# Optimization experiments

Hardware: AMD Instinct MI355X
Metric: run time of the kernel (lower is better)

The kernel has to match this reference:

```python
import jax, jax.numpy as jnp
import numpy as np

D = 256      # channels / model dim
HEADS = 8
DK = 32
DV = 32
B, H, W = 8, 32, 32
EPS = 1e-5


def setup_inputs() -> dict:
    key = jax.random.key(0)
    ks = jax.random.split(key, 9)
    s = 0.02
    return {
        "x":  jax.random.normal(ks[0], (B, D, H, W), dtype=jnp.float32),
        "Wq": jax.random.normal(ks[1], (HEADS * DK, D), dtype=jnp.float32) * s,
        "bq": jnp.zeros((HEADS * DK,), dtype=jnp.float32),
        "Wk": jax.random.normal(ks[2], (HEADS * DK, D), dtype=jnp.float32) * s,
        "bk": jnp.zeros((HEADS * DK,), dtype=jnp.float32),
        "Wv": jax.random.normal(ks[3], (HEADS * DV, D), dtype=jnp.float32) * s,
        "bv": jnp.zeros((HEADS * DV,), dtype=jnp.float32),
        "Wo": jax.random.normal(ks[4], (D, HEADS * DK), dtype=jnp.float32) * s,
        "bo": jnp.zeros((D,), dtype=jnp.float32),
    }


def reference(x, Wq, bq, Wk, bk, Wv, bv, Wo, bo):
    b, c, h, w = x.shape
    n = h * w
    # LayerNorm over [c, h, w] per sample, no affine (functional.layer_norm default)
    mu = jnp.mean(x, axis=(1, 2, 3), keepdims=True)
    var = jnp.var(x, axis=(1, 2, 3), keepdims=True)
    xn = (x - mu) * jax.lax.rsqrt(var + EPS)
    xr = xn.reshape(b, c, n).transpose(0, 2, 1)  # [b, n, c]

    def proj(Wt, bt, dh):
        y = xr @ Wt.T + bt                        # [b, n, heads*dh]
        return y.reshape(b, n, HEADS, dh).transpose(0, 2, 1, 3)  # [b, heads, n, dh]

    q = proj(Wq, bq, DK)
    k = proj(Wk, bk, DK)
    v = proj(Wv, bv, DV)

    scores = jnp.einsum('bhid,bhjd->bhij', q, k) * (DK ** -0.5)  # [b, heads, n, n]
    att = jax.nn.softmax(scores, axis=-1)
    tmp = jnp.einsum('bhij,bhjd->bhid', att, v)                  # [b, heads, n, dv]
    tmp = tmp.transpose(0, 2, 1, 3).reshape(b, n, HEADS * DV)    # [b, n, heads*dv]
    out = tmp @ Wo.T + bo                                        # [b, n, d]
    # NOTE: original does a raw .view(b, d, h, w) WITHOUT permuting — faithful reshape
    out = out.reshape(b, c, h, w)
    return out + x
```

## Files before the change

kernel.cpp:

```cpp
#include <hip/hip_runtime.h>
#include <stdint.h>

typedef unsigned short u16;
typedef unsigned int u32;
typedef __attribute__((ext_vector_type(8))) short bf16x8;
typedef __attribute__((ext_vector_type(4))) float f32x4;
typedef __attribute__((ext_vector_type(16))) float f32x16;

#define NTOK 1024
#define DMODEL 256
#define NHEAD 8
#define DK 32
#define NBATCH 8
#define PER_B (DMODEL * NTOK)

__device__ __forceinline__ float b2f(u16 h) {
    union { unsigned u; float f; } c; c.u = ((unsigned)h) << 16; return c.f;
}
__device__ __forceinline__ u16 f2b(float f) {
    unsigned u = __float_as_uint(f);
    unsigned r = u + 0x7fffu + ((u >> 16) & 1u);
    return (u16)(r >> 16);
}

__global__ void prep(const float* __restrict__ Wq, const float* __restrict__ Wk,
                     const float* __restrict__ Wv, const float* __restrict__ Wo,
                     u16* __restrict__ wb,
                     const float* __restrict__ x, float* __restrict__ part) {
    int bx = blockIdx.x;
    int t = threadIdx.x;
    if (bx < 256) {
        int m = bx >> 6;
        const float* W = (m == 0) ? Wq : (m == 1) ? Wk : (m == 2) ? Wv : Wo;
        int i = ((bx & 63) * 256 + t) * 4;
        float4 v = *(const float4*)&W[i];
        ushort4 o;
        o.x = f2b(v.x); o.y = f2b(v.y); o.z = f2b(v.z); o.w = f2b(v.w);
        *(ushort4*)&wb[m * 65536 + i] = o;
        return;
    }
    int blk = bx - 256;
    int b = blk >> 3, sl = blk & 7;
    int w = t >> 6, l = t & 63;
    const float* xb = x + (size_t)b * PER_B + sl * (PER_B / 8);
    float s = 0.f, ss = 0.f;
    for (int base = 0; base < PER_B / 8; base += 1024) {
        float4 v = *(const float4*)&xb[base + t * 4];
        s += v.x + v.y + v.z + v.w;
        ss += v.x * v.x + v.y * v.y + v.z * v.z + v.w * v.w;
    }
    for (int d = 1; d < 64; d <<= 1) {
        s += __shfl_xor(s, d, 64);
        ss += __shfl_xor(ss, d, 64);
    }
    __shared__ float red[2][4];
    if (l == 0) { red[0][w] = s; red[1][w] = ss; }
    __syncthreads();
    if (t == 0) {
        float S = red[0][0] + red[0][1] + red[0][2] + red[0][3];
        float SS = red[1][0] + red[1][1] + red[1][2] + red[1][3];
        part[(b * 8 + sl) * 2] = S;
        part[(b * 8 + sl) * 2 + 1] = SS;
    }
}

__global__ void normT(const float* __restrict__ x, const float* __restrict__ part,
                      u16* __restrict__ xn) {
    int b = blockIdx.z;
    int n0 = blockIdx.x * 32;
    int c0 = blockIdx.y * 32;
    int tx = threadIdx.x, ty = threadIdx.y;
    __shared__ float s_mu, s_rs;
    __shared__ float tile[32][33];
    if (tx == 0 && ty == 0) {
        float S = 0.f, SS = 0.f;
        for (int i = 0; i < 8; ++i) { S += part[(b * 8 + i) * 2]; SS += part[(b * 8 + i) * 2 + 1]; }
        float mu = S / (float)PER_B;
        float var = SS / (float)PER_B - mu * mu;
        s_mu = mu;
        s_rs = rsqrtf(var + 1e-5f);
    }
    __syncthreads();
    float mu = s_mu, rs = s_rs;
    const float* xb = x + (size_t)b * PER_B;
#pragma unroll
    for (int i = 0; i < 4; ++i) {
        int c = c0 + ty + i * 8;
        tile[ty + i * 8][tx] = (xb[c * NTOK + n0 + tx] - mu) * rs;
    }
    __syncthreads();
    u16* xnb = xn + (size_t)b * PER_B;
#pragma unroll
    for (int i = 0; i < 4; ++i) {
        int n = n0 + ty + i * 8;
        xnb[n * DMODEL + c0 + tx] = f2b(tile[tx][ty + i * 8]);
    }
}

__global__ __launch_bounds__(256, 4) void qkv_gemm(
    const u16* __restrict__ xn, const u16* __restrict__ wb,
    const float* __restrict__ bq, const float* __restrict__ bk,
    const float* __restrict__ bv,
    u16* __restrict__ qo, u16* __restrict__ ko, u16* __restrict__ vo) {
    int mt = blockIdx.x;
    int ot = blockIdx.y;
    int b = blockIdx.z;
    int sel = ot >> 2;
    int o0 = (ot & 3) * 64;
    const u16* W = wb + sel * 65536;
    const float* bias = (sel == 0) ? bq : (sel == 1) ? bk : bv;

    __shared__ u16 As[2][64][40];
    __shared__ u16 Bs[2][64][40];
    int t = threadIdx.x;
    int w = t >> 6, l = t & 63;
    int lr = t >> 2;
    int lc = (t & 3) * 8;
    int qd = l >> 4, ln = l & 15;

    const u16* xb = xn + ((size_t)b * NTOK + mt * 64) * DMODEL;

    {
        uint4 a0 = *(const uint4*)&xb[lr * DMODEL + lc];
        uint4 b0 = *(const uint4*)&W[(o0 + lr) * DMODEL + lc];
        *(uint4*)&As[0][lr][lc] = a0;
        *(uint4*)&Bs[0][lr][lc] = b0;
    }
    __syncthreads();

    f32x4 acc[4] = {};
#pragma unroll
    for (int kb = 0; kb < 8; ++kb) {
        int cur = kb & 1;
        uint4 a1, b1;
        if (kb < 7) {
            a1 = *(const uint4*)&xb[lr * DMODEL + (kb + 1) * 32 + lc];
            b1 = *(const uint4*)&W[(o0 + lr) * DMODEL + (kb + 1) * 32 + lc];
        }
        bf16x8 af = *(const bf16x8*)&As[cur][w * 16 + ln][qd * 8];
#pragma unroll
        for (int ns = 0; ns < 4; ++ns) {
            bf16x8 bf = *(const bf16x8*)&Bs[cur][ns * 16 + ln][qd * 8];
            acc[ns] = __builtin_amdgcn_mfma_f32_16x16x32_bf16(af, bf, acc[ns], 0, 0, 0);
        }
        if (kb < 7) {
            *(uint4*)&As[cur ^ 1][lr][lc] = a1;
            *(uint4*)&Bs[cur ^ 1][lr][lc] = b1;
            __syncthreads();
        }
    }
    if (sel < 2) {
        u16* outp = (sel == 0) ? qo : ko;
        float scale = (sel == 0) ? 0.25505654344884634f : 1.0f;
#pragma unroll
        for (int ns = 0; ns < 4; ++ns) {
            int o = o0 + ns * 16 + ln;
            float bias_f = bias[o];
            int head = o >> 5, d = o & 31;
#pragma unroll
            for (int r = 0; r < 4; ++r) {
                int n_row = mt * 64 + w * 16 + qd * 4 + r;
                float v = (acc[ns][r] + bias_f) * scale;
                outp[(((size_t)b * NHEAD + head) * NTOK + n_row) * DK + d] = f2b(v);
            }
        }
    } else {
        int n0 = mt * 64 + w * 16 + qd * 4;
#pragma unroll
        for (int ns = 0; ns < 4; ++ns) {
            int o = o0 + ns * 16 + ln;
            float bias_f = bias[o];
            int head = o >> 5, d = o & 31;
            ushort4 pk;
            pk.x = f2b(acc[ns][0] + bias_f);
            pk.y = f2b(acc[ns][1] + bias_f);
            pk.z = f2b(acc[ns][2] + bias_f);
            pk.w = f2b(acc[ns][3] + bias_f);
            *(ushort4*)&vo[(((size_t)b * NHEAD + head) * DK + d) * NTOK + n0] = pk;
        }
    }
}

__global__ __launch_bounds__(256, 4) void attn(
    const u16* __restrict__ qws, const u16* __restrict__ kws,
    const u16* __restrict__ vtws, u16* __restrict__ tmp) {
    int bh = blockIdx.x;
    int qp = blockIdx.y;
    int b = bh >> 3, h = bh & 7;
    const u16* Q  = qws  + (size_t)bh * NTOK * DK;
    const u16* K  = kws  + (size_t)bh * NTOK * DK;
    const u16* Vt = vtws + (size_t)bh * DK * NTOK;

    __shared__ float xl[2][64];
    __shared__ float xo[2][64][17];

    int t = threadIdx.x;
    int w = t >> 6, l = t & 63;
    int qsub = w >> 1, khalf = w & 1;
    int l31 = l & 31, hi = l >> 5;
    int kperm = (l31 & 19) | ((l31 & 4) << 1) | ((l31 & 8) >> 1);

    int q0 = qp * 64 + qsub * 32;
    int kb0 = khalf * 512;

    bf16x8 qf0 = *(const bf16x8*)&Q[(q0 + l31) * DK + hi * 8];
    bf16x8 qf1 = *(const bf16x8*)&Q[(q0 + l31) * DK + 16 + hi * 8];

    const u16* kp = K + (size_t)(kb0 + kperm) * DK + hi * 8;
    const u16* vp = Vt + (size_t)l31 * NTOK + kb0 + hi * 8;

    f32x16 oacc = {};
    float lsum = 0.f;

    bf16x8 kf0 = *(const bf16x8*)&kp[0];
    bf16x8 kf1 = *(const bf16x8*)&kp[16];
    bf16x8 va  = *(const bf16x8*)&vp[0];
    bf16x8 vb  = *(const bf16x8*)&vp[16];

#pragma unroll
    for (int kt = 0; kt < 16; ++kt) {
        bf16x8 nk0, nk1, nva, nvb;
        if (kt < 15) {
            const u16* kn = kp + (kt + 1) * 32 * DK;
            const u16* vn = vp + (kt + 1) * 32;
            nk0 = *(const bf16x8*)&kn[0];
            nk1 = *(const bf16x8*)&kn[16];
            nva = *(const bf16x8*)&vn[0];
            nvb = *(const bf16x8*)&vn[16];
        }
        f32x16 s = {};
        s = __builtin_amdgcn_mfma_f32_32x32x16_bf16(kf0, qf0, s, 0, 0, 0);
        s = __builtin_amdgcn_mfma_f32_32x32x16_bf16(kf1, qf1, s, 0, 0, 0);

        union { u32 u[4]; bf16x8 v; } pa, pb;
        float ps = 0.f;
#pragma unroll
        for (int j = 0; j < 4; ++j) {
            float e0 = __builtin_amdgcn_exp2f(s[2 * j]);
            float e1 = __builtin_amdgcn_exp2f(s[2 * j + 1]);
            float e2 = __builtin_amdgcn_exp2f(s[2 * j + 8]);
            float e3 = __builtin_amdgcn_exp2f(s[2 * j + 9]);
            ps += (e0 + e1) + (e2 + e3);
            pa.u[j] = __builtin_amdgcn_perm(__float_as_uint(e1), __float_as_uint(e0), 0x07060302u);
            pb.u[j] = __builtin_amdgcn_perm(__float_as_uint(e3), __float_as_uint(e2), 0x07060302u);
        }
        lsum += ps;

        oacc = __builtin_amdgcn_mfma_f32_32x32x16_bf16(va, pa.v, oacc, 0, 0, 0);
        oacc = __builtin_amdgcn_mfma_f32_32x32x16_bf16(vb, pb.v, oacc, 0, 0, 0);

        kf0 = nk0; kf1 = nk1; va = nva; vb = nvb;
    }

    if (khalf == 1) {
        xl[qsub][l] = lsum;
#pragma unroll
        for (int r = 0; r < 16; ++r) xo[qsub][l][r] = oacc[r];
    }
    __syncthreads();
    if (khalf == 0) {
        lsum += xl[qsub][l];
#pragma unroll
        for (int r = 0; r < 16; ++r) oacc[r] += xo[qsub][l][r];
        lsum += __shfl_xor(lsum, 32, 64);
        float linv = 1.0f / lsum;
        int qg = q0 + l31;
        u16* op = tmp + ((size_t)b * NTOK + qg) * DMODEL + h * DK;
#pragma unroll
        for (int g = 0; g < 4; ++g) {
            ushort4 pk;
            pk.x = f2b(oacc[g * 4 + 0] * linv);
            pk.y = f2b(oacc[g * 4 + 1] * linv);
            pk.z = f2b(oacc[g * 4 + 2] * linv);
            pk.w = f2b(oacc[g * 4 + 3] * linv);
            *(ushort4*)&op[g * 8 + hi * 4] = pk;
        }
    }
}

__global__ __launch_bounds__(256, 4) void oproj(
    const u16* __restrict__ tmp, const u16* __restrict__ wb,
    const float* __restrict__ bo, const float* __restrict__ x,
    float* __restrict__ out) {
    int mt = blockIdx.x;
    int ot = blockIdx.y;
    int b = blockIdx.z;
    const u16* Wo = wb + 3 * 65536;

    __shared__ u16 As[2][64][40];
    __shared__ u16 Bs[2][64][40];
    int t = threadIdx.x;
    int w = t >> 6, l = t & 63;
    int lr = t >> 2;
    int lc = (t & 3) * 8;
    int qd = l >> 4, ln = l & 15;

    const u16* ab = tmp + ((size_t)b * NTOK + mt * 64) * DMODEL;

    {
        uint4 a0 = *(const uint4*)&ab[lr * DMODEL + lc];
        uint4 b0 = *(const uint4*)&Wo[(ot * 64 + lr) * DMODEL + lc];
        *(uint4*)&As[0][lr][lc] = a0;
        *(uint4*)&Bs[0][lr][lc] = b0;
    }
    __syncthreads();

    f32x4 acc[4] = {};
#pragma unroll
    for (int kb = 0; kb < 8; ++kb) {
        int cur = kb & 1;
        uint4 a1, b1;
        if (kb < 7) {
            a1 = *(const uint4*)&ab[lr * DMODEL + (kb + 1) * 32 + lc];
            b1 = *(const uint4*)&Wo[(ot * 64 + lr) * DMODEL + (kb + 1) * 32 + lc];
        }
        bf16x8 af = *(const bf16x8*)&As[cur][w * 16 + ln][qd * 8];
#pragma unroll
        for (int ns = 0; ns < 4; ++ns) {
            bf16x8 bf = *(const bf16x8*)&Bs[cur][ns * 16 + ln][qd * 8];
            acc[ns] = __builtin_amdgcn_mfma_f32_16x16x32_bf16(af, bf, acc[ns], 0, 0, 0);
        }
        if (kb < 7) {
            *(uint4*)&As[cur ^ 1][lr][lc] = a1;
            *(uint4*)&Bs[cur ^ 1][lr][lc] = b1;
            __syncthreads();
        }
    }
    const float* xb = x + (size_t)b * PER_B;
    float* ob = out + (size_t)b * PER_B;
#pragma unroll
    for (int ns = 0; ns < 4; ++ns) {
        int o = ot * 64 + ns * 16 + ln;
        float bias_f = bo[o];
#pragma unroll
        for (int r = 0; r < 4; ++r) {
            int n_row = mt * 64 + w * 16 + qd * 4 + r;
            size_t idx = (size_t)n_row * DMODEL + o;
            ob[idx] = acc[ns][r] + bias_f + xb[idx];
        }
    }
}

extern "C" void kernel_launch(void* const* d_in, const int* in_sizes, int n_in,
                              void* d_out, int out_size, void* d_ws, size_t ws_size,
                              hipStream_t stream) {
    const float* x  = (const float*)d_in[0];
    const float* Wq = (const float*)d_in[1];
    const float* bq = (const float*)d_in[2];
    const float* Wk = (const float*)d_in[3];
    const float* bk = (const float*)d_in[4];
    const float* Wv = (const float*)d_in[5];
    const float* bv = (const float*)d_in[6];
    const float* Wo = (const float*)d_in[7];
    const float* bo = (const float*)d_in[8];
    float* out = (float*)d_out;

    char* ws = (char*)d_ws;
    float* part = (float*)ws;
    u16* wb  = (u16*)(ws + 1024);
    u16* xn  = (u16*)(ws + 1024 + (512u << 10));
    u16* qws = (u16*)(ws + 1024 + (512u << 10) + (4u << 20));
    u16* kws = (u16*)(ws + 1024 + (512u << 10) + (8u << 20));
    u16* vws = (u16*)(ws + 1024 + (512u << 10) + (12u << 20));
    u16* tmp = xn;

    hipLaunchKernelGGL(prep, dim3(320), dim3(256), 0, stream, Wq, Wk, Wv, Wo, wb, x, part);
    hipLaunchKernelGGL(normT, dim3(32, 8, 8), dim3(32, 8), 0, stream, x, part, xn);
    hipLaunchKernelGGL(qkv_gemm, dim3(16, 12, 8), dim3(256), 0, stream,
                       xn, wb, bq, bk, bv, qws, kws, vws);
    hipLaunchKernelGGL(attn, dim3(64, 16), dim3(256), 0, stream, qws, kws, vws, tmp);
    hipLaunchKernelGGL(oproj, dim3(16, 4, 8), dim3(256), 0, stream, tmp, wb, bo, x, out);
}
```

Baseline: 125.1 us.

## Store K and V in fragment-ordered panels for contiguous attention loads

The projection kernel now writes K and V into a panel layout that matches the MFMA fragment order, with the key permutation applied at write time. Each lane's bf16x8 load in the attention loop then reads contiguous 16-byte chunks, so a wavefront's load is fully coalesced instead of strided across rows. The explicit register double-buffered prefetch is dropped in favour of plain loads in a fully unrolled loop, leaving load scheduling to the compiler. K stores become scattered 2-byte writes in the projection epilogue, which may cost more there.

```diff
diff --git a/kernel.cpp b/kernel.cpp
--- a/kernel.cpp
+++ b/kernel.cpp
@@ -149,9 +149,8 @@
             __syncthreads();
         }
     }
-    if (sel < 2) {
-        u16* outp = (sel == 0) ? qo : ko;
-        float scale = (sel == 0) ? 0.25505654344884634f : 1.0f;
+    if (sel == 0) {
+        const float scale = 0.25505654344884634f;
 #pragma unroll
         for (int ns = 0; ns < 4; ++ns) {
             int o = o0 + ns * 16 + ln;
@@ -161,11 +160,30 @@
             for (int r = 0; r < 4; ++r) {
                 int n_row = mt * 64 + w * 16 + qd * 4 + r;
                 float v = (acc[ns][r] + bias_f) * scale;
-                outp[(((size_t)b * NHEAD + head) * NTOK + n_row) * DK + d] = f2b(v);
+                qo[(((size_t)b * NHEAD + head) * NTOK + n_row) * DK + d] = f2b(v);
+            }
+        }
+    } else if (sel == 1) {
+#pragma unroll
+        for (int ns = 0; ns < 4; ++ns) {
+            int o = o0 + ns * 16 + ln;
+            float bias_f = bias[o];
+            int head = o >> 5, d = o & 31;
+            int dh = d >> 4, h8 = (d >> 3) & 1, j = d & 7;
+            size_t base = (size_t)(b * NHEAD + head) * 32768;
+#pragma unroll
+            for (int r = 0; r < 4; ++r) {
+                int n_row = mt * 64 + w * 16 + qd * 4 + r;
+                int c = n_row >> 5, w5 = n_row & 31;
+                int kslot = (w5 & 19) | ((w5 & 4) << 1) | ((w5 & 8) >> 1);
+                float v = acc[ns][r] + bias_f;
+                ko[base + ((size_t)((c * 2 + dh) * 2 + h8)) * 256 + kslot * 8 + j] = f2b(v);
             }
         }
     } else {
         int n0 = mt * 64 + w * 16 + qd * 4;
+        int c = n0 >> 5, w5 = n0 & 31;
+        int grp = (w5 >> 4) & 1, h8 = (w5 >> 3) & 1, j = w5 & 7;
 #pragma unroll
         for (int ns = 0; ns < 4; ++ns) {
             int o = o0 + ns * 16 + ln;
@@ -176,20 +194,21 @@
             pk.y = f2b(acc[ns][1] + bias_f);
             pk.z = f2b(acc[ns][2] + bias_f);
             pk.w = f2b(acc[ns][3] + bias_f);
-            *(ushort4*)&vo[(((size_t)b * NHEAD + head) * DK + d) * NTOK + n0] = pk;
+            size_t base = (size_t)(b * NHEAD + head) * 32768;
+            *(ushort4*)&vo[base + ((size_t)((c * 2 + grp) * 2 + h8)) * 256 + d * 8 + j] = pk;
         }
     }
 }
 
 __global__ __launch_bounds__(256, 4) void attn(
-    const u16* __restrict__ qws, const u16* __restrict__ kws,
-    const u16* __restrict__ vtws, u16* __restrict__ tmp) {
+    const u16* __restrict__ qws, const u16* __restrict__ kpan,
+    const u16* __restrict__ vpan, u16* __restrict__ tmp) {
     int bh = blockIdx.x;
     int qp = blockIdx.y;
     int b = bh >> 3, h = bh & 7;
-    const u16* Q  = qws  + (size_t)bh * NTOK * DK;
-    const u16* K  = kws  + (size_t)bh * NTOK * DK;
-    const u16* Vt = vtws + (size_t)bh * DK * NTOK;
+    const u16* Q  = qws + (size_t)bh * NTOK * DK;
+    const u16* Kp = kpan + (size_t)bh * 32768;
+    const u16* Vp = vpan + (size_t)bh * 32768;
 
     __shared__ float xl[2][64];
     __shared__ float xo[2][64][17];
@@ -198,36 +217,26 @@
     int w = t >> 6, l = t & 63;
     int qsub = w >> 1, khalf = w & 1;
     int l31 = l & 31, hi = l >> 5;
-    int kperm = (l31 & 19) | ((l31 & 4) << 1) | ((l31 & 8) >> 1);
 
     int q0 = qp * 64 + qsub * 32;
-    int kb0 = khalf * 512;
+    int c0 = khalf * 16;
 
     bf16x8 qf0 = *(const bf16x8*)&Q[(q0 + l31) * DK + hi * 8];
     bf16x8 qf1 = *(const bf16x8*)&Q[(q0 + l31) * DK + 16 + hi * 8];
 
-    const u16* kp = K + (size_t)(kb0 + kperm) * DK + hi * 8;
-    const u16* vp = Vt + (size_t)l31 * NTOK + kb0 + hi * 8;
+    const u16* kb = Kp + (size_t)c0 * 1024 + hi * 256 + l31 * 8;
+    const u16* vb = Vp + (size_t)c0 * 1024 + hi * 256 + l31 * 8;
 
     f32x16 oacc = {};
     float lsum = 0.f;
 
-    bf16x8 kf0 = *(const bf16x8*)&kp[0];
-    bf16x8 kf1 = *(const bf16x8*)&kp[16];
-    bf16x8 va  = *(const bf16x8*)&vp[0];
-    bf16x8 vb  = *(const bf16x8*)&vp[16];
-
-#pragma unroll
-    for (int kt = 0; kt < 16; ++kt) {
-        bf16x8 nk0, nk1, nva, nvb;
-        if (kt < 15) {
-            const u16* kn = kp + (kt + 1) * 32 * DK;
-            const u16* vn = vp + (kt + 1) * 32;
-            nk0 = *(const bf16x8*)&kn[0];
-            nk1 = *(const bf16x8*)&kn[16];
-            nva = *(const bf16x8*)&vn[0];
-            nvb = *(const bf16x8*)&vn[16];
-        }
+#pragma unroll
+    for (int c = 0; c < 16; ++c) {
+        bf16x8 kf0 = *(const bf16x8*)&kb[c * 1024];
+        bf16x8 kf1 = *(const bf16x8*)&kb[c * 1024 + 512];
+        bf16x8 va  = *(const bf16x8*)&vb[c * 1024];
+        bf16x8 vg  = *(const bf16x8*)&vb[c * 1024 + 512];
+
         f32x16 s = {};
         s = __builtin_amdgcn_mfma_f32_32x32x16_bf16(kf0, qf0, s, 0, 0, 0);
         s = __builtin_amdgcn_mfma_f32_32x32x16_bf16(kf1, qf1, s, 0, 0, 0);
@@ -247,9 +256,7 @@
         lsum += ps;
 
         oacc = __builtin_amdgcn_mfma_f32_32x32x16_bf16(va, pa.v, oacc, 0, 0, 0);
-        oacc = __builtin_amdgcn_mfma_f32_32x32x16_bf16(vb, pb.v, oacc, 0, 0, 0);
-
-        kf0 = nk0; kf1 = nk1; va = nva; vb = nvb;
+        oacc = __builtin_amdgcn_mfma_f32_32x32x16_bf16(vg, pb.v, oacc, 0, 0, 0);
     }
 
     if (khalf == 1) {
```

After: 115.2 us. 7.9% less time.
